# Kernel optimization log

Hardware: AMD Instinct MI355X
Metric: run time of the kernel (lower is better)

The kernel has to match this reference:

```python
import jax, jax.numpy as jnp
import numpy as np

D_MODEL = 1024
NUM_HEADS = 16
D_K = D_MODEL // NUM_HEADS
LN_EPS = 1e-5


def setup_inputs() -> dict:
    key = jax.random.key(0)
    ks = jax.random.split(key, 9)
    s = 1.0 / np.sqrt(D_MODEL)
    x = jax.random.normal(ks[0], (4, 2048, D_MODEL), dtype=jnp.float32)
    Wq = jax.random.uniform(ks[1], (D_MODEL, D_MODEL), minval=-s, maxval=s, dtype=jnp.float32)
    bq = jax.random.uniform(ks[2], (D_MODEL,), minval=-s, maxval=s, dtype=jnp.float32)
    Wk = jax.random.uniform(ks[3], (D_MODEL, D_MODEL), minval=-s, maxval=s, dtype=jnp.float32)
    bk = jax.random.uniform(ks[4], (D_MODEL,), minval=-s, maxval=s, dtype=jnp.float32)
    Wv = jax.random.uniform(ks[5], (D_MODEL, D_MODEL), minval=-s, maxval=s, dtype=jnp.float32)
    bv = jax.random.uniform(ks[6], (D_MODEL,), minval=-s, maxval=s, dtype=jnp.float32)
    Wo = jax.random.uniform(ks[7], (D_MODEL, D_MODEL), minval=-s, maxval=s, dtype=jnp.float32)
    bo = jax.random.uniform(ks[8], (D_MODEL,), minval=-s, maxval=s, dtype=jnp.float32)
    gamma = jnp.ones((D_MODEL,), dtype=jnp.float32)
    beta = jnp.zeros((D_MODEL,), dtype=jnp.float32)
    return {"x": x, "Wq": Wq, "bq": bq, "Wk": Wk, "bk": bk, "Wv": Wv, "bv": bv,
            "Wo": Wo, "bo": bo, "gamma": gamma, "beta": beta}


def reference(x, Wq, bq, Wk, bk, Wv, bv, Wo, bo, gamma, beta):
    B, S, D = x.shape
    H, dk = NUM_HEADS, D_K
    # torch Linear: y = x @ W^T + b; split heads -> (B, H, S, dk)
    def proj(W, b):
        return (jnp.einsum('bsd,ed->bse', x, W) + b).reshape(B, S, H, dk).transpose(0, 2, 1, 3)
    Q = proj(Wq, bq)
    K = proj(Wk, bk)
    V = proj(Wv, bv)
    scores = jnp.einsum('bhqd,bhkd->bhqk', Q, K) / jnp.sqrt(jnp.float32(dk))
    attn = jax.nn.softmax(scores, axis=-1)  # dropout is identity in eval mode
    ctx = jnp.einsum('bhqk,bhkd->bhqd', attn, V)
    ctx = ctx.transpose(0, 2, 1, 3).reshape(B, S, D)
    out = jnp.einsum('bsd,ed->bse', ctx, Wo) + bo
    y = out + x
    mu = jnp.mean(y, axis=-1, keepdims=True)
    var = jnp.mean(jnp.square(y - mu), axis=-1, keepdims=True)
    return (y - mu) * jax.lax.rsqrt(var + LN_EPS) * gamma + beta
```

## Files before the change

### kernel.cpp

```cpp
#include <hip/hip_runtime.h>


#define SEQ 2048
#define DMODEL 1024
#define NH 16
#define DK 64
#define NROWS 8192

typedef unsigned short u16;
typedef unsigned int u32;
typedef __bf16 bf16;
typedef bf16 bf16x2 __attribute__((ext_vector_type(2)));
typedef bf16 bf16x8 __attribute__((ext_vector_type(8)));
typedef float f32x4 __attribute__((ext_vector_type(4)));
typedef float f32x16 __attribute__((ext_vector_type(16)));
typedef unsigned u32x2 __attribute__((ext_vector_type(2)));

__device__ inline u16 bfbits(float f) { return __builtin_bit_cast(u16, (bf16)f); }
__device__ inline u32 packbf2(float a, float b) {
    return (u32)bfbits(a) | ((u32)bfbits(b) << 16);
}

__device__ inline float sexp2(float s) {
    return __builtin_bit_cast(float, (u32)(int)fmaf(s, 8388608.0f, 1064986823.0f));
}

__device__ inline void gload16(const u16* g, u16* l) {
    __builtin_amdgcn_global_load_lds(
        (const __attribute__((address_space(1))) u32*)g,
        (__attribute__((address_space(3))) u32*)l, 16, 0, 0);
}

__device__ inline void plswap(u32& a, u32& b) {
#if __has_builtin(__builtin_amdgcn_permlane32_swap)
    u32x2 r = __builtin_amdgcn_permlane32_swap(a, b, false, false);
    a = r[0]; b = r[1];
#else
    u32 xa = __shfl_xor(a, 32), xb = __shfl_xor(b, 32);
    int hi = (threadIdx.x & 63) >> 5;
    u32 na = hi ? xb : a;
    u32 nb = hi ? b : xa;
    a = na; b = nb;
#endif
}

__global__ __launch_bounds__(256) void cvt_all(
    const float* __restrict__ x,  const float* __restrict__ w0,
    const float* __restrict__ w1, const float* __restrict__ w2,
    const float* __restrict__ w3,
    u16* __restrict__ xo, u16* __restrict__ o0, u16* __restrict__ o1,
    u16* __restrict__ o2, u16* __restrict__ o3) {
    const int b = blockIdx.x;
    const float* in;
    u16* out;
    int base;
    if (b < 8192) {
        in = x; out = xo; base = b << 10;
    } else {
        const int wsel = (b - 8192) >> 10;
        base = ((b - 8192) & 1023) << 10;
        switch (wsel) {
            case 0: in = w0; out = o0; break;
            case 1: in = w1; out = o1; break;
            case 2: in = w2; out = o2; break;
            default: in = w3; out = o3; break;
        }
    }
    const int i = base + threadIdx.x * 4;
    float4 v = *(const float4*)(in + i);
    ushort4 o;
    o.x = bfbits(v.x); o.y = bfbits(v.y); o.z = bfbits(v.z); o.w = bfbits(v.w);
    *(ushort4*)(out + i) = o;
}

template <int EPI>
__global__ __launch_bounds__(512) void gemm_piped(
    const u16* __restrict__ A, const u16* __restrict__ Bm,
    const float* __restrict__ bias0, const float* __restrict__ bias1,
    const float* __restrict__ bias2,
    u16* __restrict__ Qo, u16* __restrict__ Ko, u16* __restrict__ Vo,
    const float* __restrict__ xres, float* __restrict__ yout) {
    __shared__ __align__(16) u16 smem[32768];

    const int tid  = threadIdx.x;
    const int lane = tid & 63;
    const int w    = tid >> 6;
    const int wr   = (w >> 1) * 32;
    const int wc   = (w & 1) * 64;
    const int l16  = lane & 15;
    const int lq   = lane >> 4;
    const int m0   = blockIdx.x * 128;
    const int n0   = blockIdx.y * 128;

    f32x4 acc[2][4];
#pragma unroll
    for (int m = 0; m < 2; m++)
#pragma unroll
        for (int n = 0; n < 4; n++) {
            f32x4 z = {0.f, 0.f, 0.f, 0.f};
            acc[m][n] = z;
        }

    const int l8r = lane >> 3;
    const int sch = (lane & 7) ^ l8r;
    const u16* a_g = A  + (size_t)(m0 + w * 8 + l8r) * 1024 + sch * 8;
    const u16* b_g = Bm + (size_t)(n0 + w * 8 + l8r) * 1024 + sch * 8;
    u16* asd = smem + w * 512;
    u16* bsd = smem + 16384 + w * 512;

#define STAGE(kt, c) do {                                              \
        gload16(a_g + (kt) * 64,         asd + (c) * 8192);            \
        gload16(a_g + 65536 + (kt) * 64, asd + (c) * 8192 + 4096);     \
        gload16(b_g + (kt) * 64,         bsd + (c) * 8192);            \
        gload16(b_g + 65536 + (kt) * 64, bsd + (c) * 8192 + 4096);     \
    } while (0)

    STAGE(0, 0);
    STAGE(1, 1);

    for (int kt = 0; kt < 16; kt++) {
        const int cur = kt & 1;
        if (kt < 15) asm volatile("s_waitcnt vmcnt(4)" ::: "memory");
        else         asm volatile("s_waitcnt vmcnt(0)" ::: "memory");
        __builtin_amdgcn_s_barrier();

        const u16* Asl = smem + cur * 8192;
        const u16* Bsl = smem + 16384 + cur * 8192;
#pragma unroll
        for (int kk = 0; kk < 2; kk++) {
            bf16x8 af[2], bfr[4];
#pragma unroll
            for (int m = 0; m < 2; m++)
                af[m] = *(const bf16x8*)&Asl[(wr + m * 16 + l16) * 64 +
                                             (((kk << 2) | lq) ^ (l16 & 7)) * 8];
#pragma unroll
            for (int n = 0; n < 4; n++)
                bfr[n] = *(const bf16x8*)&Bsl[(wc + n * 16 + l16) * 64 +
                                              (((kk << 2) | lq) ^ (l16 & 7)) * 8];
            __builtin_amdgcn_s_setprio(1);
#pragma unroll
            for (int m = 0; m < 2; m++)
#pragma unroll
                for (int n = 0; n < 4; n++)
                    acc[m][n] = __builtin_amdgcn_mfma_f32_16x16x32_bf16(
                        af[m], bfr[n], acc[m][n], 0, 0, 0);
            __builtin_amdgcn_s_setprio(0);
        }
        __builtin_amdgcn_s_barrier();
        if (kt < 14) STAGE(kt + 2, cur);
    }
#undef STAGE

    if (EPI == 0 && n0 >= 2048) {
        const int e0 = n0 - 2048;
#pragma unroll
        for (int m = 0; m < 2; m++)
#pragma unroll
            for (int n = 0; n < 4; n++) {
                const int col = wc + n * 16 + l16;
                const int row = wr + lq * 4 + m * 16;
                const float bias = bias2[e0 + col];
                ushort4 pk;
                pk.x = bfbits(acc[m][n][0] + bias);
                pk.y = bfbits(acc[m][n][1] + bias);
                pk.z = bfbits(acc[m][n][2] + bias);
                pk.w = bfbits(acc[m][n][3] + bias);
                *(ushort4*)&smem[col * 128 + (row ^ ((col & 7) << 3))] = pk;
            }
        __syncthreads();
        const int b = m0 >> 11;
        const int sbase = m0 & 2047;
#pragma unroll
        for (int i = 0; i < 4; i++) {
            const int c = tid + 512 * i;
            const int col = c >> 4;
            const int s0 = (c & 15) * 8;
            uint4 val = *(const uint4*)&smem[col * 128 + (s0 ^ ((col & 7) << 3))];
            const int eg = e0 + col;
            const int bh = b * NH + (eg >> 6);
            *(uint4*)&Vo[((size_t)bh * DK + (eg & 63)) * SEQ + sbase + s0] = val;
        }
        return;
    }

    const int rbase = m0 + wr + lq * 4;
#pragma unroll
    for (int m = 0; m < 2; m++)
#pragma unroll
        for (int n = 0; n < 4; n++) {
            if (EPI == 0) {
                const int which = n0 >> 10;
                const int e = (n0 & 1023) + wc + n * 16 + l16;
                const float bias = (which == 0) ? bias0[e] : bias1[e];
                const int h = e >> 6, d = e & 63;
#pragma unroll
                for (int r = 0; r < 4; r++) {
                    const int row = rbase + m * 16 + r;
                    float v = acc[m][n][r] + bias;
                    if (which == 0) v *= 0.18033688011112042f;
                    const int b = row >> 11, s = row & 2047;
                    const int bh = b * NH + h;
                    if (which == 0)
                        Qo[((size_t)bh * SEQ + s) * DK + d] = bfbits(v);
                    else
                        Ko[((size_t)bh * SEQ + s) * DK + d] = bfbits(v);
                }
            } else {
                const int col = n0 + wc + n * 16 + l16;
#pragma unroll
                for (int r = 0; r < 4; r++) {
                    const int row = rbase + m * 16 + r;
                    float v = acc[m][n][r] + bias0[col] + xres[(size_t)row * DMODEL + col];
                    yout[(size_t)row * DMODEL + col] = v;
                }
            }
        }
}

__global__ __launch_bounds__(512) void attn(const u16* __restrict__ Qb,
                                            const u16* __restrict__ Kb,
                                            const u16* __restrict__ Vtb,
                                            u16* __restrict__ ctx) {
    __shared__ __align__(16) u16 smem[16384];

    const int tid  = threadIdx.x;
    const int lane = tid & 63;
    const int w    = tid >> 6;
    const int q    = lane & 31;
    const int hi   = lane >> 5;
    const int bh   = blockIdx.x;
    const int q0   = blockIdx.y * 256 + w * 32;

    const u16* qp = Qb + ((size_t)bh * SEQ + q0 + q) * DK + hi * 8;
    bf16x8 qf0 = *(const bf16x8*)(qp);
    bf16x8 qf1 = *(const bf16x8*)(qp + 16);
    bf16x8 qf2 = *(const bf16x8*)(qp + 32);
    bf16x8 qf3 = *(const bf16x8*)(qp + 48);

    const int l8r = lane >> 3;
    const int sch = (lane & 7) ^ l8r;
    const u16* kg = Kb  + ((size_t)bh * SEQ + w * 8 + l8r) * 64 + sch * 8;
    const u16* vg = Vtb + ((size_t)bh * DK  + w * 8 + l8r) * SEQ + sch * 8;
    u16* kl = smem + w * 512;
    u16* vl = smem + 8192 + w * 512;

    f32x16 oacc0, oacc1;
#pragma unroll
    for (int r = 0; r < 16; r++) { oacc0[r] = 0.f; oacc1[r] = 0.f; }
    f32x16 fzero;
#pragma unroll
    for (int r = 0; r < 16; r++) fzero[r] = 0.f;
    float la = 0.f, lb = 0.f;

#if __has_builtin(__builtin_amdgcn_fdot2_f32_bf16)
    bf16x2 ones2;
    ones2[0] = (bf16)1.0f; ones2[1] = (bf16)1.0f;
#endif

    gload16(kg, kl);
    gload16(vg, vl);
    __syncthreads();

    for (int t = 0; t < SEQ / 64; t++) {
        if (t < SEQ / 64 - 1) {
            gload16(kg + (size_t)(t + 1) * 4096, kl + ((t + 1) & 1) * 4096);
            gload16(vg + (size_t)(t + 1) * 64,  vl + ((t + 1) & 1) * 4096);
        }
        const u16* Kl = smem + (t & 1) * 4096;
        const u16* Vl = smem + 8192 + (t & 1) * 4096;

        f32x16 sacc0, sacc1;
        {
            bf16x8 k00 = *(const bf16x8*)&Kl[(q)      * 64 + ((0 | hi) ^ (q & 7)) * 8];
            bf16x8 k01 = *(const bf16x8*)&Kl[(q)      * 64 + ((2 | hi) ^ (q & 7)) * 8];
            bf16x8 k02 = *(const bf16x8*)&Kl[(q)      * 64 + ((4 | hi) ^ (q & 7)) * 8];
            bf16x8 k03 = *(const bf16x8*)&Kl[(q)      * 64 + ((6 | hi) ^ (q & 7)) * 8];
            bf16x8 k10 = *(const bf16x8*)&Kl[(q + 32) * 64 + ((0 | hi) ^ (q & 7)) * 8];
            bf16x8 k11 = *(const bf16x8*)&Kl[(q + 32) * 64 + ((2 | hi) ^ (q & 7)) * 8];
            bf16x8 k12 = *(const bf16x8*)&Kl[(q + 32) * 64 + ((4 | hi) ^ (q & 7)) * 8];
            bf16x8 k13 = *(const bf16x8*)&Kl[(q + 32) * 64 + ((6 | hi) ^ (q & 7)) * 8];
            __builtin_amdgcn_s_setprio(1);
            sacc0 = __builtin_amdgcn_mfma_f32_32x32x16_bf16(k00, qf0, fzero, 0, 0, 0);
            sacc1 = __builtin_amdgcn_mfma_f32_32x32x16_bf16(k10, qf0, fzero, 0, 0, 0);
            sacc0 = __builtin_amdgcn_mfma_f32_32x32x16_bf16(k01, qf1, sacc0, 0, 0, 0);
            sacc1 = __builtin_amdgcn_mfma_f32_32x32x16_bf16(k11, qf1, sacc1, 0, 0, 0);
            sacc0 = __builtin_amdgcn_mfma_f32_32x32x16_bf16(k02, qf2, sacc0, 0, 0, 0);
            sacc1 = __builtin_amdgcn_mfma_f32_32x32x16_bf16(k12, qf2, sacc1, 0, 0, 0);
            sacc0 = __builtin_amdgcn_mfma_f32_32x32x16_bf16(k03, qf3, sacc0, 0, 0, 0);
            sacc1 = __builtin_amdgcn_mfma_f32_32x32x16_bf16(k13, qf3, sacc1, 0, 0, 0);
            __builtin_amdgcn_s_setprio(0);
        }

#pragma unroll
        for (int r = 0; r < 16; r++) sacc0[r] = sexp2(sacc0[r]);
#pragma unroll
        for (int r = 0; r < 16; r++) sacc1[r] = sexp2(sacc1[r]);

        u32 wa[8], wb[8];
#pragma unroll
        for (int i = 0; i < 8; i++) wa[i] = packbf2(sacc0[2 * i], sacc0[2 * i + 1]);
#pragma unroll
        for (int i = 0; i < 8; i++) wb[i] = packbf2(sacc1[2 * i], sacc1[2 * i + 1]);

#if __has_builtin(__builtin_amdgcn_fdot2_f32_bf16)
#pragma unroll
        for (int i = 0; i < 8; i++)
            la = __builtin_amdgcn_fdot2_f32_bf16(
                __builtin_bit_cast(bf16x2, wa[i]), ones2, la, false);
#pragma unroll
        for (int i = 0; i < 8; i++)
            lb = __builtin_amdgcn_fdot2_f32_bf16(
                __builtin_bit_cast(bf16x2, wb[i]), ones2, lb, false);
#else
        {
            float s0 = ((sacc0[0] + sacc0[1]) + (sacc0[2] + sacc0[3])) +
                       ((sacc0[4] + sacc0[5]) + (sacc0[6] + sacc0[7]));
            float s1 = ((sacc0[8] + sacc0[9]) + (sacc0[10] + sacc0[11])) +
                       ((sacc0[12] + sacc0[13]) + (sacc0[14] + sacc0[15]));
            float s2 = ((sacc1[0] + sacc1[1]) + (sacc1[2] + sacc1[3])) +
                       ((sacc1[4] + sacc1[5]) + (sacc1[6] + sacc1[7]));
            float s3 = ((sacc1[8] + sacc1[9]) + (sacc1[10] + sacc1[11])) +
                       ((sacc1[12] + sacc1[13]) + (sacc1[14] + sacc1[15]));
            la += (s0 + s1);
            lb += (s2 + s3);
        }
#endif

        plswap(wa[0], wa[2]); plswap(wa[1], wa[3]);
        plswap(wa[4], wa[6]); plswap(wa[5], wa[7]);
        plswap(wb[0], wb[2]); plswap(wb[1], wb[3]);
        plswap(wb[4], wb[6]); plswap(wb[5], wb[7]);
        union { u32 u[4]; bf16x8 v; } pf0, pf1, pf2, pf3;
        pf0.u[0] = wa[0]; pf0.u[1] = wa[1]; pf0.u[2] = wa[2]; pf0.u[3] = wa[3];
        pf1.u[0] = wa[4]; pf1.u[1] = wa[5]; pf1.u[2] = wa[6]; pf1.u[3] = wa[7];
        pf2.u[0] = wb[0]; pf2.u[1] = wb[1]; pf2.u[2] = wb[2]; pf2.u[3] = wb[3];
        pf3.u[0] = wb[4]; pf3.u[1] = wb[5]; pf3.u[2] = wb[6]; pf3.u[3] = wb[7];

        {
            bf16x8 v00 = *(const bf16x8*)&Vl[(q)      * 64 + ((0 | hi) ^ (q & 7)) * 8];
            bf16x8 v01 = *(const bf16x8*)&Vl[(q)      * 64 + ((2 | hi) ^ (q & 7)) * 8];
            bf16x8 v02 = *(const bf16x8*)&Vl[(q)      * 64 + ((4 | hi) ^ (q & 7)) * 8];
            bf16x8 v03 = *(const bf16x8*)&Vl[(q)      * 64 + ((6 | hi) ^ (q & 7)) * 8];
            bf16x8 v10 = *(const bf16x8*)&Vl[(q + 32) * 64 + ((0 | hi) ^ (q & 7)) * 8];
            bf16x8 v11 = *(const bf16x8*)&Vl[(q + 32) * 64 + ((2 | hi) ^ (q & 7)) * 8];
            bf16x8 v12 = *(const bf16x8*)&Vl[(q + 32) * 64 + ((4 | hi) ^ (q & 7)) * 8];
            bf16x8 v13 = *(const bf16x8*)&Vl[(q + 32) * 64 + ((6 | hi) ^ (q & 7)) * 8];
            __builtin_amdgcn_s_setprio(1);
            oacc0 = __builtin_amdgcn_mfma_f32_32x32x16_bf16(v00, pf0.v, oacc0, 0, 0, 0);
            oacc1 = __builtin_amdgcn_mfma_f32_32x32x16_bf16(v10, pf0.v, oacc1, 0, 0, 0);
            oacc0 = __builtin_amdgcn_mfma_f32_32x32x16_bf16(v01, pf1.v, oacc0, 0, 0, 0);
            oacc1 = __builtin_amdgcn_mfma_f32_32x32x16_bf16(v11, pf1.v, oacc1, 0, 0, 0);
            oacc0 = __builtin_amdgcn_mfma_f32_32x32x16_bf16(v02, pf2.v, oacc0, 0, 0, 0);
            oacc1 = __builtin_amdgcn_mfma_f32_32x32x16_bf16(v12, pf2.v, oacc1, 0, 0, 0);
            oacc0 = __builtin_amdgcn_mfma_f32_32x32x16_bf16(v03, pf3.v, oacc0, 0, 0, 0);
            oacc1 = __builtin_amdgcn_mfma_f32_32x32x16_bf16(v13, pf3.v, oacc1, 0, 0, 0);
            __builtin_amdgcn_s_setprio(0);
        }

        __syncthreads();
    }

    float l_ = la + lb;
    const float lfull = l_ + __shfl_xor(l_, 32);
    const float invl = 1.f / lfull;
    const int wbase = w * 2048;
#pragma unroll
    for (int r = 0; r < 16; r++) {
        const int dk0 = (r & 3) + 8 * (r >> 2) + 4 * hi;
        const int dk1 = 32 + dk0;
        smem[wbase + q * 64 + (((dk0 >> 3) ^ (q & 7)) << 3) + (dk0 & 7)] = bfbits(oacc0[r] * invl);
        smem[wbase + q * 64 + (((dk1 >> 3) ^ (q & 7)) << 3) + (dk1 & 7)] = bfbits(oacc1[r] * invl);
    }
    __syncthreads();
    const int b = bh >> 4, h = bh & 15;
    const int r4 = lane >> 1;
    const int cc = (lane & 1) * 4;
#pragma unroll
    for (int c = 0; c < 4; c++) {
        const int chunk = cc + c;
        uint4 val = *(const uint4*)&smem[wbase + r4 * 64 + ((chunk ^ (r4 & 7)) << 3)];
        *(uint4*)&ctx[((size_t)(b * SEQ + q0 + r4)) * DMODEL + h * DK + chunk * 8] = val;
    }
}

__global__ __launch_bounds__(256) void ln_inplace(float* __restrict__ y,
                                                  const float* __restrict__ gamma,
                                                  const float* __restrict__ beta) {
    const int row = blockIdx.x;
    float* p = y + (size_t)row * DMODEL;
    const int tid = threadIdx.x;
    float4 v = *(const float4*)(p + tid * 4);
    float s  = v.x + v.y + v.z + v.w;
    float sq = v.x * v.x + v.y * v.y + v.z * v.z + v.w * v.w;
#pragma unroll
    for (int m = 1; m < 64; m <<= 1) {
        s  += __shfl_xor(s, m);
        sq += __shfl_xor(sq, m);
    }
    __shared__ float rs[4], rq[4];
    if ((tid & 63) == 0) { rs[tid >> 6] = s; rq[tid >> 6] = sq; }
    __syncthreads();
    s  = rs[0] + rs[1] + rs[2] + rs[3];
    sq = rq[0] + rq[1] + rq[2] + rq[3];
    const float mean = s * (1.0f / 1024.0f);
    const float var  = sq * (1.0f / 1024.0f) - mean * mean;
    const float inv  = rsqrtf(var + 1e-5f);
    const int c = tid * 4;
    float4 g4 = *(const float4*)(gamma + c);
    float4 b4 = *(const float4*)(beta + c);
    float4 o;
    o.x = (v.x - mean) * inv * g4.x + b4.x;
    o.y = (v.y - mean) * inv * g4.y + b4.y;
    o.z = (v.z - mean) * inv * g4.z + b4.z;
    o.w = (v.w - mean) * inv * g4.w + b4.w;
    *(float4*)(p + c) = o;
}

extern "C" void kernel_launch(void* const* d_in, const int* in_sizes, int n_in,
                              void* d_out, int out_size, void* d_ws, size_t ws_size,
                              hipStream_t stream) {
    const float* x     = (const float*)d_in[0];
    const float* Wq    = (const float*)d_in[1];
    const float* bq    = (const float*)d_in[2];
    const float* Wk    = (const float*)d_in[3];
    const float* bk    = (const float*)d_in[4];
    const float* Wv    = (const float*)d_in[5];
    const float* bv    = (const float*)d_in[6];
    const float* Wo    = (const float*)d_in[7];
    const float* bo    = (const float*)d_in[8];
    const float* gamma = (const float*)d_in[9];
    const float* beta  = (const float*)d_in[10];
    float* out = (float*)d_out;

    u16* x_bf    = (u16*)d_ws;
    u16* Wqkv_bf = x_bf + (size_t)NROWS * DMODEL;
    u16* Wo_bf   = Wqkv_bf + (size_t)3072 * 1024;
    u16* Q_bf    = Wo_bf + (size_t)1024 * 1024;
    u16* K_bf    = Q_bf + (size_t)64 * SEQ * DK;
    u16* Vt_bf   = K_bf + (size_t)64 * SEQ * DK;
    u16* ctx_bf  = x_bf;

    cvt_all<<<12288, 256, 0, stream>>>(x, Wq, Wk, Wv, Wo,
                                       x_bf, Wqkv_bf, Wqkv_bf + 1048576,
                                       Wqkv_bf + 2097152, Wo_bf);

    gemm_piped<0><<<dim3(64, 24), 512, 0, stream>>>(x_bf, Wqkv_bf,
                                                    bq, bk, bv, Q_bf, K_bf, Vt_bf,
                                                    nullptr, nullptr);
    attn<<<dim3(64, 8), 512, 0, stream>>>(Q_bf, K_bf, Vt_bf, ctx_bf);
    gemm_piped<1><<<dim3(64, 8), 512, 0, stream>>>(ctx_bf, Wo_bf,
                                                   bo, nullptr, nullptr,
                                                   nullptr, nullptr, nullptr,
                                                   x, out);
    ln_inplace<<<8192, 256, 0, stream>>>(out, gamma, beta);
}
```

Before: 185.8 us.

## Triple-buffer K/V tiles in attention with explicit vmcnt waits and one barrier

The attention kernel's K/V staging in shared memory goes from double to triple buffering. Tiles are prefetched two iterations ahead, and each iteration waits on the vector-memory counter with a single barrier in place of two __syncthreads. The goal is to hide more global-load latency behind the MFMA work and cut barrier overhead. In exchange, LDS use per block rises from 32KB to 48KB, which could lower occupancy, and correctness now rests on the hand-set vmcnt counts matching how gload16 issues its loads.

Measured after the change: 186.8 us. About the same (+0.5%).

```diff
diff --git a/kernel.cpp b/kernel.cpp
--- a/kernel.cpp
+++ b/kernel.cpp
@@ -221,7 +221,7 @@
                                             const u16* __restrict__ Kb,
                                             const u16* __restrict__ Vtb,
                                             u16* __restrict__ ctx) {
-    __shared__ __align__(16) u16 smem[16384];
+    __shared__ __align__(16) u16 smem[24576];
 
     const int tid  = threadIdx.x;
     const int lane = tid & 63;
@@ -241,8 +241,8 @@
     const int sch = (lane & 7) ^ l8r;
     const u16* kg = Kb  + ((size_t)bh * SEQ + w * 8 + l8r) * 64 + sch * 8;
     const u16* vg = Vtb + ((size_t)bh * DK  + w * 8 + l8r) * SEQ + sch * 8;
-    u16* kl = smem + w * 512;
-    u16* vl = smem + 8192 + w * 512;
+    u16* kld = smem + w * 512;
+    u16* vld = smem + 12288 + w * 512;
 
     f32x16 oacc0, oacc1;
 #pragma unroll
@@ -257,17 +257,24 @@
     ones2[0] = (bf16)1.0f; ones2[1] = (bf16)1.0f;
 #endif
 
-    gload16(kg, kl);
-    gload16(vg, vl);
-    __syncthreads();
-
+#define ASTAGE(t, b) do {                                   \
+        gload16(kg + (size_t)(t) * 4096, kld + (b) * 4096); \
+        gload16(vg + (size_t)(t) * 64,   vld + (b) * 4096); \
+    } while (0)
+
+    ASTAGE(0, 0);
+    ASTAGE(1, 1);
+
+    int cur = 0;
+    int nx2 = 2;
     for (int t = 0; t < SEQ / 64; t++) {
-        if (t < SEQ / 64 - 1) {
-            gload16(kg + (size_t)(t + 1) * 4096, kl + ((t + 1) & 1) * 4096);
-            gload16(vg + (size_t)(t + 1) * 64,  vl + ((t + 1) & 1) * 4096);
-        }
-        const u16* Kl = smem + (t & 1) * 4096;
-        const u16* Vl = smem + 8192 + (t & 1) * 4096;
+        if (t < SEQ / 64 - 1) asm volatile("s_waitcnt vmcnt(2)" ::: "memory");
+        else                  asm volatile("s_waitcnt vmcnt(0)" ::: "memory");
+        __builtin_amdgcn_s_barrier();
+        if (t < SEQ / 64 - 2) ASTAGE(t + 2, nx2);
+
+        const u16* Kl = smem + cur * 4096;
+        const u16* Vl = smem + 12288 + cur * 4096;
 
         f32x16 sacc0, sacc1;
         {
@@ -357,8 +364,12 @@
             __builtin_amdgcn_s_setprio(0);
         }
 
-        __syncthreads();
-    }
+        cur = (cur == 2) ? 0 : cur + 1;
+        nx2 = (nx2 == 2) ? 0 : nx2 + 1;
+    }
+#undef ASTAGE
+
+    __syncthreads();
 
     float l_ = la + lb;
     const float lfull = l_ + __shfl_xor(l_, 32);
```

## Fuse LayerNorm into output projection GEMM via grid-wide barrier

Applied to the files above, without the earlier changes.

Splits the templated GEMM into a QKV kernel and an output-projection kernel that applies bias, residual and LayerNorm in its epilogue. Per-row partial sums and squared sums are written to a workspace, then an atomic spin barrier across all 512 blocks is followed by the final normalisation. This removes the separate LN kernel and a round trip of the fp32 output through memory. It adds a memset launch and a grid-wide spin wait that assumes all 512 blocks are co-resident, so it could deadlock or stall if they are not.

New measurement: 256.3 us. 37.9% more time.

```diff
diff --git a/kernel.cpp b/kernel.cpp
--- a/kernel.cpp
+++ b/kernel.cpp
@@ -73,13 +73,11 @@
     *(ushort4*)(out + i) = o;
 }
 
-template <int EPI>
-__global__ __launch_bounds__(512) void gemm_piped(
+__global__ __launch_bounds__(512) void gemm_qkv(
     const u16* __restrict__ A, const u16* __restrict__ Bm,
     const float* __restrict__ bias0, const float* __restrict__ bias1,
     const float* __restrict__ bias2,
-    u16* __restrict__ Qo, u16* __restrict__ Ko, u16* __restrict__ Vo,
-    const float* __restrict__ xres, float* __restrict__ yout) {
+    u16* __restrict__ Qo, u16* __restrict__ Ko, u16* __restrict__ Vo) {
     __shared__ __align__(16) u16 smem[32768];
 
     const int tid  = threadIdx.x;
@@ -151,7 +149,7 @@
     }
 #undef STAGE
 
-    if (EPI == 0 && n0 >= 2048) {
+    if (n0 >= 2048) {
         const int e0 = n0 - 2048;
 #pragma unroll
         for (int m = 0; m < 2; m++)
@@ -188,31 +186,178 @@
     for (int m = 0; m < 2; m++)
 #pragma unroll
         for (int n = 0; n < 4; n++) {
-            if (EPI == 0) {
-                const int which = n0 >> 10;
-                const int e = (n0 & 1023) + wc + n * 16 + l16;
-                const float bias = (which == 0) ? bias0[e] : bias1[e];
-                const int h = e >> 6, d = e & 63;
-#pragma unroll
-                for (int r = 0; r < 4; r++) {
-                    const int row = rbase + m * 16 + r;
-                    float v = acc[m][n][r] + bias;
-                    if (which == 0) v *= 0.18033688011112042f;
-                    const int b = row >> 11, s = row & 2047;
-                    const int bh = b * NH + h;
-                    if (which == 0)
-                        Qo[((size_t)bh * SEQ + s) * DK + d] = bfbits(v);
-                    else
-                        Ko[((size_t)bh * SEQ + s) * DK + d] = bfbits(v);
-                }
-            } else {
-                const int col = n0 + wc + n * 16 + l16;
-#pragma unroll
-                for (int r = 0; r < 4; r++) {
-                    const int row = rbase + m * 16 + r;
-                    float v = acc[m][n][r] + bias0[col] + xres[(size_t)row * DMODEL + col];
-                    yout[(size_t)row * DMODEL + col] = v;
-                }
+            const int which = n0 >> 10;
+            const int e = (n0 & 1023) + wc + n * 16 + l16;
+            const float bias = (which == 0) ? bias0[e] : bias1[e];
+            const int h = e >> 6, d = e & 63;
+#pragma unroll
+            for (int r = 0; r < 4; r++) {
+                const int row = rbase + m * 16 + r;
+                float v = acc[m][n][r] + bias;
+                if (which == 0) v *= 0.18033688011112042f;
+                const int b = row >> 11, s = row & 2047;
+                const int bh = b * NH + h;
+                if (which == 0)
+                    Qo[((size_t)bh * SEQ + s) * DK + d] = bfbits(v);
+                else
+                    Ko[((size_t)bh * SEQ + s) * DK + d] = bfbits(v);
+            }
+        }
+}
+
+__global__ __launch_bounds__(512) void gemm_o_ln(
+    const u16* __restrict__ A, const u16* __restrict__ Bm,
+    const float* __restrict__ bias, const float* __restrict__ xres,
+    const float* __restrict__ gamma, const float* __restrict__ beta,
+    float* __restrict__ gpart, u32* __restrict__ gbar,
+    float* __restrict__ yout) {
+    __shared__ __align__(16) u16 smem[32768];
+
+    const int tid  = threadIdx.x;
+    const int lane = tid & 63;
+    const int w    = tid >> 6;
+    const int wr   = (w >> 1) * 32;
+    const int wc   = (w & 1) * 64;
+    const int l16  = lane & 15;
+    const int lq   = lane >> 4;
+    const int m0   = blockIdx.x * 128;
+    const int n0   = blockIdx.y * 128;
+
+    f32x4 acc[2][4];
+#pragma unroll
+    for (int m = 0; m < 2; m++)
+#pragma unroll
+        for (int n = 0; n < 4; n++) {
+            f32x4 z = {0.f, 0.f, 0.f, 0.f};
+            acc[m][n] = z;
+        }
+
+    const int l8r = lane >> 3;
+    const int sch = (lane & 7) ^ l8r;
+    const u16* a_g = A  + (size_t)(m0 + w * 8 + l8r) * 1024 + sch * 8;
+    const u16* b_g = Bm + (size_t)(n0 + w * 8 + l8r) * 1024 + sch * 8;
+    u16* asd = smem + w * 512;
+    u16* bsd = smem + 16384 + w * 512;
+
+#define STAGE(kt, c) do {                                              \
+        gload16(a_g + (kt) * 64,         asd + (c) * 8192);            \
+        gload16(a_g + 65536 + (kt) * 64, asd + (c) * 8192 + 4096);     \
+        gload16(b_g + (kt) * 64,         bsd + (c) * 8192);            \
+        gload16(b_g + 65536 + (kt) * 64, bsd + (c) * 8192 + 4096);     \
+    } while (0)
+
+    STAGE(0, 0);
+    STAGE(1, 1);
+
+    for (int kt = 0; kt < 16; kt++) {
+        const int cur = kt & 1;
+        if (kt < 15) asm volatile("s_waitcnt vmcnt(4)" ::: "memory");
+        else         asm volatile("s_waitcnt vmcnt(0)" ::: "memory");
+        __builtin_amdgcn_s_barrier();
+
+        const u16* Asl = smem + cur * 8192;
+        const u16* Bsl = smem + 16384 + cur * 8192;
+#pragma unroll
+        for (int kk = 0; kk < 2; kk++) {
+            bf16x8 af[2], bfr[4];
+#pragma unroll
+            for (int m = 0; m < 2; m++)
+                af[m] = *(const bf16x8*)&Asl[(wr + m * 16 + l16) * 64 +
+                                             (((kk << 2) | lq) ^ (l16 & 7)) * 8];
+#pragma unroll
+            for (int n = 0; n < 4; n++)
+                bfr[n] = *(const bf16x8*)&Bsl[(wc + n * 16 + l16) * 64 +
+                                              (((kk << 2) | lq) ^ (l16 & 7)) * 8];
+            __builtin_amdgcn_s_setprio(1);
+#pragma unroll
+            for (int m = 0; m < 2; m++)
+#pragma unroll
+                for (int n = 0; n < 4; n++)
+                    acc[m][n] = __builtin_amdgcn_mfma_f32_16x16x32_bf16(
+                        af[m], bfr[n], acc[m][n], 0, 0, 0);
+            __builtin_amdgcn_s_setprio(0);
+        }
+        __builtin_amdgcn_s_barrier();
+        if (kt < 14) STAGE(kt + 2, cur);
+    }
+#undef STAGE
+
+#pragma unroll
+    for (int m = 0; m < 2; m++)
+#pragma unroll
+        for (int n = 0; n < 4; n++) {
+            const int col = n0 + wc + n * 16 + l16;
+            const float bv = bias[col];
+#pragma unroll
+            for (int r = 0; r < 4; r++) {
+                const int row = m0 + wr + lq * 4 + m * 16 + r;
+                acc[m][n][r] += bv + xres[(size_t)row * DMODEL + col];
+            }
+        }
+
+    float* sbuf = (float*)smem;
+    float* qbuf = sbuf + 256;
+#pragma unroll
+    for (int m = 0; m < 2; m++)
+#pragma unroll
+        for (int r = 0; r < 4; r++) {
+            float s  = (acc[m][0][r] + acc[m][1][r]) + (acc[m][2][r] + acc[m][3][r]);
+            float qq = (acc[m][0][r] * acc[m][0][r] + acc[m][1][r] * acc[m][1][r]) +
+                       (acc[m][2][r] * acc[m][2][r] + acc[m][3][r] * acc[m][3][r]);
+#pragma unroll
+            for (int k = 1; k < 16; k <<= 1) {
+                s  += __shfl_xor(s, k);
+                qq += __shfl_xor(qq, k);
+            }
+            if (l16 == 0) {
+                const int rl = wr + lq * 4 + m * 16 + r;
+                sbuf[rl * 2 + (w & 1)] = s;
+                qbuf[rl * 2 + (w & 1)] = qq;
+            }
+        }
+    __syncthreads();
+    if (tid < 128) {
+        float* gp = gpart + ((size_t)(m0 + tid)) * 16 + blockIdx.y * 2;
+        gp[0] = sbuf[tid * 2] + sbuf[tid * 2 + 1];
+        gp[1] = qbuf[tid * 2] + qbuf[tid * 2 + 1];
+    }
+
+    __syncthreads();
+    if (tid == 0) {
+        __threadfence();
+        __hip_atomic_fetch_add(gbar, 1u, __ATOMIC_ACQ_REL, __HIP_MEMORY_SCOPE_AGENT);
+        while (__hip_atomic_load(gbar, __ATOMIC_ACQUIRE, __HIP_MEMORY_SCOPE_AGENT) < 512u) {
+            __builtin_amdgcn_s_sleep(8);
+        }
+        __threadfence();
+    }
+    __syncthreads();
+
+    float* meanb = sbuf;
+    float* invb  = sbuf + 128;
+    if (tid < 128) {
+        const float* gp = gpart + ((size_t)(m0 + tid)) * 16;
+        float s  = 0.f, qq = 0.f;
+#pragma unroll
+        for (int nb = 0; nb < 8; nb++) { s += gp[nb * 2]; qq += gp[nb * 2 + 1]; }
+        const float mean = s * (1.0f / 1024.0f);
+        const float var  = qq * (1.0f / 1024.0f) - mean * mean;
+        meanb[tid] = mean;
+        invb[tid]  = rsqrtf(var + 1e-5f);
+    }
+    __syncthreads();
+#pragma unroll
+    for (int m = 0; m < 2; m++)
+#pragma unroll
+        for (int n = 0; n < 4; n++) {
+            const int col = n0 + wc + n * 16 + l16;
+            const float g = gamma[col];
+            const float bb = beta[col];
+#pragma unroll
+            for (int r = 0; r < 4; r++) {
+                const int rl = wr + lq * 4 + m * 16 + r;
+                yout[(size_t)(m0 + rl) * DMODEL + col] =
+                    (acc[m][n][r] - meanb[rl]) * invb[rl] * g + bb;
             }
         }
 }
@@ -383,39 +528,6 @@
     }
 }
 
-__global__ __launch_bounds__(256) void ln_inplace(float* __restrict__ y,
-                                                  const float* __restrict__ gamma,
-                                                  const float* __restrict__ beta) {
-    const int row = blockIdx.x;
-    float* p = y + (size_t)row * DMODEL;
-    const int tid = threadIdx.x;
-    float4 v = *(const float4*)(p + tid * 4);
-    float s  = v.x + v.y + v.z + v.w;
-    float sq = v.x * v.x + v.y * v.y + v.z * v.z + v.w * v.w;
-#pragma unroll
-    for (int m = 1; m < 64; m <<= 1) {
-        s  += __shfl_xor(s, m);
-        sq += __shfl_xor(sq, m);
-    }
-    __shared__ float rs[4], rq[4];
-    if ((tid & 63) == 0) { rs[tid >> 6] = s; rq[tid >> 6] = sq; }
-    __syncthreads();
-    s  = rs[0] + rs[1] + rs[2] + rs[3];
-    sq = rq[0] + rq[1] + rq[2] + rq[3];
-    const float mean = s * (1.0f / 1024.0f);
-    const float var  = sq * (1.0f / 1024.0f) - mean * mean;
-    const float inv  = rsqrtf(var + 1e-5f);
-    const int c = tid * 4;
-    float4 g4 = *(const float4*)(gamma + c);
-    float4 b4 = *(const float4*)(beta + c);
-    float4 o;
-    o.x = (v.x - mean) * inv * g4.x + b4.x;
-    o.y = (v.y - mean) * inv * g4.y + b4.y;
-    o.z = (v.z - mean) * inv * g4.z + b4.z;
-    o.w = (v.w - mean) * inv * g4.w + b4.w;
-    *(float4*)(p + c) = o;
-}
-
 extern "C" void kernel_launch(void* const* d_in, const int* in_sizes, int n_in,
                               void* d_out, int out_size, void* d_ws, size_t ws_size,
                               hipStream_t stream) {
@@ -439,18 +551,18 @@
     u16* K_bf    = Q_bf + (size_t)64 * SEQ * DK;
     u16* Vt_bf   = K_bf + (size_t)64 * SEQ * DK;
     u16* ctx_bf  = x_bf;
+    float* gpart = (float*)Q_bf;
+    u32*   gbar  = (u32*)(Q_bf + 262144);
 
     cvt_all<<<12288, 256, 0, stream>>>(x, Wq, Wk, Wv, Wo,
                                        x_bf, Wqkv_bf, Wqkv_bf + 1048576,
                                        Wqkv_bf + 2097152, Wo_bf);
 
-    gemm_piped<0><<<dim3(64, 24), 512, 0, stream>>>(x_bf, Wqkv_bf,
-                                                    bq, bk, bv, Q_bf, K_bf, Vt_bf,
-                                                    nullptr, nullptr);
+    gemm_qkv<<<dim3(64, 24), 512, 0, stream>>>(x_bf, Wqkv_bf,
+                                               bq, bk, bv, Q_bf, K_bf, Vt_bf);
     attn<<<dim3(64, 8), 512, 0, stream>>>(Q_bf, K_bf, Vt_bf, ctx_bf);
-    gemm_piped<1><<<dim3(64, 8), 512, 0, stream>>>(ctx_bf, Wo_bf,
-                                                   bo, nullptr, nullptr,
-                                                   nullptr, nullptr, nullptr,
-                                                   x, out);
-    ln_inplace<<<8192, 256, 0, stream>>>(out, gamma, beta);
-}
+
+    hipMemsetAsync(gbar, 0, sizeof(u32), stream);
+    gemm_o_ln<<<dim3(64, 8), 512, 0, stream>>>(ctx_bf, Wo_bf, bo, x,
+                                               gamma, beta, gpart, gbar, out);
+}
```
